# Kernel optimization log

Measured on AMD Instinct MI355X. Metric: run time of the kernel, lower is better.

Reference implementation:

```python
import jax, jax.numpy as jnp
import numpy as np
from jax import lax

B, D, H, W = 4, 64, 64, 64
CH = 150


def setup_inputs() -> dict:
    key = jax.random.key(0)
    k1, k2, k3, k4 = jax.random.split(key, 4)
    image = jax.random.uniform(k1, (B, 2, D, H, W), dtype=jnp.float32)
    # PyTorch-like init scales
    h_w = jax.random.normal(k2, (CH, 1, 3, 3, 3), dtype=jnp.float32) * (1.0 / np.sqrt(27.0))
    h_b = jax.random.normal(k3, (CH,), dtype=jnp.float32) * 0.05
    p_w = jax.random.normal(k4, (1, CH, 1, 1, 1), dtype=jnp.float32) * (1.0 / np.sqrt(CH))
    return {"image": image, "h_w": h_w, "h_b": h_b, "p_w": p_w, "k": 30}


def _max_pool3(v):
    # 3x3x3 max pool, stride 1, padding 1 (torch pads with -inf for max pool)
    return lax.reduce_window(
        v, -jnp.inf, lax.max,
        window_dimensions=(1, 1, 3, 3, 3),
        window_strides=(1, 1, 1, 1, 1),
        padding=[(0, 0), (0, 0), (1, 1), (1, 1), (1, 1)])


def reference(image, h_w, h_b, p_w, k):
    x = image[:, 0:1]            # [B,1,D,H,W] occupancy
    r = image[:, 1:2]            # [B,1,D,H,W] reward
    h = lax.conv_general_dilated(
        x, h_w, window_strides=(1, 1, 1), padding="SAME",
        dimension_numbers=("NCDHW", "OIDHW", "NCDHW"))
    h = jax.nn.relu(h + h_b[None, :, None, None, None])  # [B,150,D,H,W]
    # 1x1x1 conv == channel contraction
    p = jax.nn.sigmoid(jnp.einsum("bcdhw,c->bdhw", h, p_w[0, :, 0, 0, 0])[:, None])
    v = r
    for _ in range(k):
        v = jnp.maximum(v, r + p * (_max_pool3(v) - r))
    return v
```

## Files before the change

kernel.cpp:

```cpp
#include <hip/hip_runtime.h>
#include <math.h>

#define NEG_INF (-__builtin_inff())

typedef __attribute__((ext_vector_type(8))) short short8;
typedef __attribute__((ext_vector_type(4))) float f32x4;

__device__ __forceinline__ unsigned f2bf(float f) {
    union { float f; unsigned u; } v; v.f = f;
    return (v.u + 0x7fffu + ((v.u >> 16) & 1u)) >> 16;
}

__device__ __forceinline__ float dpp_shr1(float x) {
    return __int_as_float(__builtin_amdgcn_update_dpp(
        0, __float_as_int(x), 0x111, 0xF, 0xF, true));
}
__device__ __forceinline__ float dpp_shr2(float x) {
    return __int_as_float(__builtin_amdgcn_update_dpp(
        0, __float_as_int(x), 0x112, 0xF, 0xF, true));
}
__device__ __forceinline__ float dpp_shr4(float x) {
    return __int_as_float(__builtin_amdgcn_update_dpp(
        0, __float_as_int(x), 0x114, 0xF, 0xF, true));
}
__device__ __forceinline__ float dpp_shr8(float x) {
    return __int_as_float(__builtin_amdgcn_update_dpp(
        0, __float_as_int(x), 0x118, 0xF, 0xF, true));
}
__device__ __forceinline__ float dpp_shl1(float x) {
    return __int_as_float(__builtin_amdgcn_update_dpp(
        0, __float_as_int(x), 0x101, 0xF, 0xF, true));
}

__global__ __launch_bounds__(256) void pad_kernel(
    const float* __restrict__ img, unsigned short* __restrict__ pad)
{
    int i = blockIdx.x * 256 + threadIdx.x;
    if (i >= 66 * 66 * 66) return;
    int b = blockIdx.y;
    int z = i / 4356;
    int rem = i - z * 4356;
    int y = rem / 66;
    int x = rem - y * 66;
    float v = 0.f;
    if (z >= 1 && z <= 64 && y >= 1 && y <= 64 && x >= 1 && x <= 64)
        v = img[((size_t)b << 19) + ((z - 1) << 12) + ((y - 1) << 6) + (x - 1)];
    pad[(size_t)b * 287496 + i] = (unsigned short)f2bf(v);
}

__global__ __launch_bounds__(256, 4) void gate_mfma(
    const unsigned short* __restrict__ pad,
    const float* __restrict__ hw, const float* __restrict__ hb,
    const float* __restrict__ pw, float* __restrict__ p)
{
    __shared__ int4 Bsh[10 * 64];

    const int lane = threadIdx.x & 63;
    const int col  = lane & 15;
    const int q    = lane >> 4;
    const int wid  = threadIdx.x >> 6;
    const int W    = blockIdx.x * 4 + wid;

    for (int t = wid; t < 10; t += 4) {
        int c = 16 * t + col;
        bool cv = c < 150;
        unsigned hv[8];
        #pragma unroll
        for (int j = 0; j < 8; ++j) {
            int k = 8 * q + j;
            float wv = 0.f;
            if (cv) {
                if (k < 27) wv = hw[c * 27 + k];
                else if (k == 27) wv = hb[c];
            }
            hv[j] = f2bf(wv);
        }
        Bsh[t * 64 + lane] = make_int4(hv[0] | (hv[1] << 16), hv[2] | (hv[3] << 16),
                                       hv[4] | (hv[5] << 16), hv[6] | (hv[7] << 16));
    }
    float pwv[10];
    #pragma unroll
    for (int t = 0; t < 10; ++t) {
        int c = 16 * t + col;
        pwv[t] = (c < 150) ? pw[c] : 0.f;
    }
    __syncthreads();

    int4 bfrag[10];
    #pragma unroll
    for (int t = 0; t < 10; ++t) bfrag[t] = Bsh[t * 64 + lane];

    int offL[8]; unsigned cstA[8]; bool ldA[8];
    #pragma unroll
    for (int j = 0; j < 8; ++j) {
        int k = 8 * q + j;
        int dz = (k * 57) >> 9;
        int rem = k - 9 * dz;
        int dy = (rem * 171) >> 9;
        int dx = rem - 3 * dy;
        ldA[j]  = (k < 27);
        offL[j] = (k < 27) ? (dz * 4356 + dy * 66 + dx) : 0;
        cstA[j] = (k == 27) ? 0x3F80u : 0u;
    }

    int y = W & 63, zz = (W >> 6) & 63, b = W >> 12;
    int rbase = b * 287496 + zz * 4356 + y * 66 + col;

    #pragma unroll 2
    for (int i = 0; i < 4; ++i) {
        int x0    = i << 4;
        int abase = rbase + x0;

        unsigned av[8];
        #pragma unroll
        for (int j = 0; j < 8; ++j) {
            unsigned v = pad[abase + offL[j]];
            av[j] = ldA[j] ? v : cstA[j];
        }
        union { int4 i4; short8 s8; } af, bfu;
        af.i4 = make_int4(av[0] | (av[1] << 16), av[2] | (av[3] << 16),
                          av[4] | (av[5] << 16), av[6] | (av[7] << 16));

        const f32x4 zero = {0.f, 0.f, 0.f, 0.f};
        f32x4 rr[10];
        #pragma unroll
        for (int t = 0; t < 10; ++t) {
            bfu.i4 = bfrag[t];
            rr[t] = __builtin_amdgcn_mfma_f32_16x16x32_bf16(af.s8, bfu.s8, zero, 0, 0, 0);
        }
        float ax = 0.f, ay = 0.f, az = 0.f, aw = 0.f;
        #pragma unroll
        for (int t = 0; t < 10; ++t) {
            ax = fmaf(pwv[t], fmaxf(rr[t].x, 0.f), ax);
            ay = fmaf(pwv[t], fmaxf(rr[t].y, 0.f), ay);
            az = fmaf(pwv[t], fmaxf(rr[t].z, 0.f), az);
            aw = fmaf(pwv[t], fmaxf(rr[t].w, 0.f), aw);
        }
        ax += dpp_shr1(ax); ax += dpp_shr2(ax); ax += dpp_shr4(ax); ax += dpp_shr8(ax);
        ay += dpp_shr1(ay); ay += dpp_shr2(ay); ay += dpp_shr4(ay); ay += dpp_shr8(ay);
        az += dpp_shr1(az); az += dpp_shr2(az); az += dpp_shr4(az); az += dpp_shr8(az);
        aw += dpp_shr1(aw); aw += dpp_shr2(aw); aw += dpp_shr4(aw); aw += dpp_shr8(aw);
        if (col == 15) {
            float4 o;
            o.x = 1.f / (1.f + __expf(-ax));
            o.y = 1.f / (1.f + __expf(-ay));
            o.z = 1.f / (1.f + __expf(-az));
            o.w = 1.f / (1.f + __expf(-aw));
            *(float4*)(p + (b << 18) + (zz << 12) + (y << 6) + x0 + 4 * q) = o;
        }
    }
}

#define YC2 14
#define PL2 896
#define HALF 5

template<int T>
__global__ __launch_bounds__(448, 3) void prop_kernel(
    const float* __restrict__ vin, int sstride,
    const float* __restrict__ rimg,
    const float* __restrict__ pbuf,
    float* __restrict__ vout)
{
    __shared__ float TL[8 * PL2];
    __shared__ float VEX[2 * PL2];

    int blk = blockIdx.x;
    int b  = blk >> 7;
    int tz = ((blk >> 3) & 15) << 2;
    int ty = (blk & 7) << 3;

    const float* vb = vin  + (size_t)b * sstride;
    const float* rb = rimg + ((size_t)b << 19);
    const float* pb = pbuf + ((size_t)b << 18);
    float*       ob = vout + ((size_t)b << 18);

    int tid  = threadIdx.x;
    int h    = (tid >= 224);
    int t2   = tid - h * 224;
    int x4   = t2 & 15, x0 = x4 << 2;
    int yy   = t2 >> 4;

    int gy = ty + yy - 3;
    bool vy = (unsigned)gy < 64u;
    int lbase = yy * 64 + x0;
    int goff  = gy * 64 + x0;

    float4 v[HALF];
    #pragma unroll
    for (int zi = 0; zi < HALF; ++zi) {
        int z  = h ? (9 - zi) : zi;
        int gz = tz + z - 3;
        float4 val = make_float4(NEG_INF, NEG_INF, NEG_INF, NEG_INF);
        if (vy && ((unsigned)gz < 64u)) val = *(const float4*)(vb + (gz << 12) + goff);
        v[zi] = val;
    }
    *(float4*)(VEX + h * PL2 + lbase) = v[HALF - 1];
    __syncthreads();

    #pragma unroll
    for (int it = 0; it < T; ++it) {
        const int lo = 4 - T + it;
        bool act_t = (yy >= lo - 1) && (yy < 15 - lo);
        bool act   = (yy >= lo) && (yy < YC2 - lo);

        float4 vexN = *(const float4*)(VEX + (h ^ 1) * PL2 + lbase);
        float4 t[4];
        #pragma unroll
        for (int zi = lo; zi < HALF; ++zi) {
            float4 za = v[zi - 1];
            float4 zb = v[zi];
            float4 zc = (zi == HALF - 1) ? vexN : v[zi + 1];
            float4 zm;
            zm.x = fmaxf(fmaxf(za.x, zb.x), zc.x);
            zm.y = fmaxf(fmaxf(za.y, zb.y), zc.y);
            zm.z = fmaxf(fmaxf(za.z, zb.z), zc.z);
            zm.w = fmaxf(fmaxf(za.w, zb.w), zc.w);
            float lm = dpp_shr1(zm.w);
            float rm = dpp_shl1(zm.x);
            if (x4 == 0)  lm = NEG_INF;
            if (x4 == 15) rm = NEG_INF;
            float4 tt;
            tt.x = fmaxf(lm, fmaxf(zm.x, zm.y));
            tt.y = fmaxf(zm.x, fmaxf(zm.y, zm.z));
            tt.z = fmaxf(zm.y, fmaxf(zm.z, zm.w));
            tt.w = fmaxf(fmaxf(zm.z, zm.w), rm);
            t[zi - lo] = tt;
            int z = h ? (9 - zi) : zi;
            if (act_t) *(float4*)(TL + (z - 1) * PL2 + lbase) = tt;
        }
        __syncthreads();

        #pragma unroll
        for (int zi = lo; zi < HALF; ++zi) {
            int z  = h ? (9 - zi) : zi;
            int gz = tz + z - 3;
            if (act) {
                const float* tp = TL + (z - 1) * PL2 + lbase;
                float4 tu = *(const float4*)(tp - 64);
                float4 td = *(const float4*)(tp + 64);
                float4 ts = t[zi - lo];
                float4 m3;
                m3.x = fmaxf(fmaxf(tu.x, td.x), ts.x);
                m3.y = fmaxf(fmaxf(tu.y, td.y), ts.y);
                m3.z = fmaxf(fmaxf(tu.z, td.z), ts.z);
                m3.w = fmaxf(fmaxf(tu.w, td.w), ts.w);
                if (vy && ((unsigned)gz < 64u)) {
                    int off = (gz << 12) + goff;
                    float4 pv = *(const float4*)(pb + off);
                    float4 rv = *(const float4*)(rb + off);
                    float4 nv;
                    nv.x = fmaxf(v[zi].x, fmaf(pv.x, m3.x - rv.x, rv.x));
                    nv.y = fmaxf(v[zi].y, fmaf(pv.y, m3.y - rv.y, rv.y));
                    nv.z = fmaxf(v[zi].z, fmaf(pv.z, m3.z - rv.z, rv.z));
                    nv.w = fmaxf(v[zi].w, fmaf(pv.w, m3.w - rv.w, rv.w));
                    v[zi] = nv;
                    if (it == T - 1) *(float4*)(ob + off) = nv;
                }
            }
        }
        *(float4*)(VEX + h * PL2 + lbase) = v[HALF - 1];
        __syncthreads();
    }
}

extern "C" void kernel_launch(void* const* d_in, const int* in_sizes, int n_in,
                              void* d_out, int out_size, void* d_ws, size_t ws_size,
                              hipStream_t stream) {
    const float* img = (const float*)d_in[0];
    const float* hw  = (const float*)d_in[1];
    const float* hb  = (const float*)d_in[2];
    const float* pw  = (const float*)d_in[3];

    float* out = (float*)d_out;
    float* p   = (float*)d_ws;
    float* vA  = (float*)((char*)d_ws + (4u << 20));
    unsigned short* pad = (unsigned short*)((char*)d_ws + (4u << 20));

    pad_kernel<<<dim3(1124, 4), 256, 0, stream>>>(img, pad);
    gate_mfma<<<4096, 256, 0, stream>>>(pad, hw, hb, pw, p);

    const float* r0 = img + (1 << 18);

    prop_kernel<3><<<512, 448, 0, stream>>>(r0,  1 << 19, r0, p, vA);
    prop_kernel<3><<<512, 448, 0, stream>>>(vA,  1 << 18, r0, p, out);
    prop_kernel<3><<<512, 448, 0, stream>>>(out, 1 << 18, r0, p, vA);
    prop_kernel<3><<<512, 448, 0, stream>>>(vA,  1 << 18, r0, p, out);
    prop_kernel<3><<<512, 448, 0, stream>>>(out, 1 << 18, r0, p, vA);
    prop_kernel<3><<<512, 448, 0, stream>>>(vA,  1 << 18, r0, p, out);
    prop_kernel<3><<<512, 448, 0, stream>>>(out, 1 << 18, r0, p, vA);
    prop_kernel<3><<<512, 448, 0, stream>>>(vA,  1 << 18, r0, p, out);
    prop_kernel<3><<<512, 448, 0, stream>>>(out, 1 << 18, r0, p, vA);
    prop_kernel<3><<<512, 448, 0, stream>>>(vA,  1 << 18, r0, p, out);
}
```

Before: 179.0 us.

## Replace inter-half z exchange with redundant halo compute and double-buffered tiles

```diff
diff --git a/kernel.cpp b/kernel.cpp
--- a/kernel.cpp
+++ b/kernel.cpp
@@ -153,17 +153,16 @@
 
 #define YC2 14
 #define PL2 896
-#define HALF 5
+#define TLP (8 * PL2)
 
 template<int T>
-__global__ __launch_bounds__(448, 3) void prop_kernel(
+__global__ __launch_bounds__(448, 2) void prop_kernel(
     const float* __restrict__ vin, int sstride,
     const float* __restrict__ rimg,
     const float* __restrict__ pbuf,
     float* __restrict__ vout)
 {
-    __shared__ float TL[8 * PL2];
-    __shared__ float VEX[2 * PL2];
+    __shared__ float TL[2 * TLP];
 
     int blk = blockIdx.x;
     int b  = blk >> 7;
@@ -186,31 +185,30 @@
     int lbase = yy * 64 + x0;
     int goff  = gy * 64 + x0;
 
-    float4 v[HALF];
-    #pragma unroll
-    for (int zi = 0; zi < HALF; ++zi) {
+    float4 v[8];
+    #pragma unroll
+    for (int zi = 0; zi < 8; ++zi) {
         int z  = h ? (9 - zi) : zi;
         int gz = tz + z - 3;
         float4 val = make_float4(NEG_INF, NEG_INF, NEG_INF, NEG_INF);
         if (vy && ((unsigned)gz < 64u)) val = *(const float4*)(vb + (gz << 12) + goff);
         v[zi] = val;
     }
-    *(float4*)(VEX + h * PL2 + lbase) = v[HALF - 1];
-    __syncthreads();
-
+
+    int cur = 0;
     #pragma unroll
     for (int it = 0; it < T; ++it) {
-        const int lo = 4 - T + it;
+        const int lo = 1 + it;
+        const int hi = 6 - it;
         bool act_t = (yy >= lo - 1) && (yy < 15 - lo);
         bool act   = (yy >= lo) && (yy < YC2 - lo);
 
-        float4 vexN = *(const float4*)(VEX + (h ^ 1) * PL2 + lbase);
-        float4 t[4];
-        #pragma unroll
-        for (int zi = lo; zi < HALF; ++zi) {
+        float4 t[6];
+        #pragma unroll
+        for (int zi = lo; zi <= hi; ++zi) {
             float4 za = v[zi - 1];
             float4 zb = v[zi];
-            float4 zc = (zi == HALF - 1) ? vexN : v[zi + 1];
+            float4 zc = v[zi + 1];
             float4 zm;
             zm.x = fmaxf(fmaxf(za.x, zb.x), zc.x);
             zm.y = fmaxf(fmaxf(za.y, zb.y), zc.y);
@@ -225,21 +223,23 @@
             tt.y = fmaxf(zm.x, fmaxf(zm.y, zm.z));
             tt.z = fmaxf(zm.y, fmaxf(zm.z, zm.w));
             tt.w = fmaxf(fmaxf(zm.z, zm.w), rm);
-            t[zi - lo] = tt;
-            int z = h ? (9 - zi) : zi;
-            if (act_t) *(float4*)(TL + (z - 1) * PL2 + lbase) = tt;
+            t[zi - 1] = tt;
+            if (zi <= 4) {
+                int z = h ? (9 - zi) : zi;
+                if (act_t) *(float4*)(TL + cur * TLP + (z - 1) * PL2 + lbase) = tt;
+            }
         }
         __syncthreads();
 
         #pragma unroll
-        for (int zi = lo; zi < HALF; ++zi) {
+        for (int zi = lo; zi <= hi; ++zi) {
             int z  = h ? (9 - zi) : zi;
             int gz = tz + z - 3;
             if (act) {
-                const float* tp = TL + (z - 1) * PL2 + lbase;
+                const float* tp = TL + cur * TLP + (z - 1) * PL2 + lbase;
                 float4 tu = *(const float4*)(tp - 64);
                 float4 td = *(const float4*)(tp + 64);
-                float4 ts = t[zi - lo];
+                float4 ts = t[zi - 1];
                 float4 m3;
                 m3.x = fmaxf(fmaxf(tu.x, td.x), ts.x);
                 m3.y = fmaxf(fmaxf(tu.y, td.y), ts.y);
@@ -259,8 +259,7 @@
                 }
             }
         }
-        *(float4*)(VEX + h * PL2 + lbase) = v[HALF - 1];
-        __syncthreads();
+        cur ^= 1;
     }
 }
 
```

New measurement: 184.5 us. +3.1%, slower.

## Fold projection weights into conv weights with sign-sorted channels in gate kernel

Applied to the files above, without the earlier changes.

```diff
diff --git a/kernel.cpp b/kernel.cpp
--- a/kernel.cpp
+++ b/kernel.cpp
@@ -14,18 +14,6 @@
 __device__ __forceinline__ float dpp_shr1(float x) {
     return __int_as_float(__builtin_amdgcn_update_dpp(
         0, __float_as_int(x), 0x111, 0xF, 0xF, true));
-}
-__device__ __forceinline__ float dpp_shr2(float x) {
-    return __int_as_float(__builtin_amdgcn_update_dpp(
-        0, __float_as_int(x), 0x112, 0xF, 0xF, true));
-}
-__device__ __forceinline__ float dpp_shr4(float x) {
-    return __int_as_float(__builtin_amdgcn_update_dpp(
-        0, __float_as_int(x), 0x114, 0xF, 0xF, true));
-}
-__device__ __forceinline__ float dpp_shr8(float x) {
-    return __int_as_float(__builtin_amdgcn_update_dpp(
-        0, __float_as_int(x), 0x118, 0xF, 0xF, true));
 }
 __device__ __forceinline__ float dpp_shl1(float x) {
     return __int_as_float(__builtin_amdgcn_update_dpp(
@@ -48,47 +36,63 @@
     pad[(size_t)b * 287496 + i] = (unsigned short)f2bf(v);
 }
 
-__global__ __launch_bounds__(256, 4) void gate_mfma(
+__global__ __launch_bounds__(256) void prep_kernel(
+    const float* __restrict__ hw, const float* __restrict__ hb,
+    const float* __restrict__ pw, int4* __restrict__ wfrag, int* __restrict__ bnp)
+{
+    __shared__ float pwl[160];
+    __shared__ int   perml[160];
+    int tid = threadIdx.x;
+    if (tid < 160) pwl[tid] = (tid < 150) ? pw[tid] : 0.f;
+    __syncthreads();
+    if (tid < 160) {
+        int Bn = 0;
+        for (int c = 0; c < 150; ++c) Bn += (pwl[c] < 0.f) ? 1 : 0;
+        if (tid == 0) bnp[0] = Bn;
+        int orig = -1;
+        if (tid < Bn) {
+            int cnt = 0;
+            for (int c = 0; c < 150; ++c) if (pwl[c] < 0.f) { if (cnt == tid) { orig = c; break; } ++cnt; }
+        } else if (tid < 150) {
+            int want = tid - Bn, cnt = 0;
+            for (int c = 0; c < 150; ++c) if (!(pwl[c] < 0.f)) { if (cnt == want) { orig = c; break; } ++cnt; }
+        }
+        perml[tid] = orig;
+    }
+    __syncthreads();
+    for (int idx = tid; idx < 640; idx += 256) {
+        int t = idx >> 6, lane = idx & 63;
+        int col = lane & 15, q = lane >> 4;
+        int s = 16 * t + col;
+        int orig = perml[s];
+        unsigned hv[8];
+        #pragma unroll
+        for (int j = 0; j < 8; ++j) {
+            int k = 8 * q + j;
+            float wv = 0.f;
+            if (orig >= 0) {
+                if (k < 27) wv = pwl[orig] * hw[orig * 27 + k];
+                else if (k == 27) wv = pwl[orig] * hb[orig];
+            }
+            hv[j] = f2bf(wv);
+        }
+        wfrag[t * 64 + lane] = make_int4(hv[0] | (hv[1] << 16), hv[2] | (hv[3] << 16),
+                                         hv[4] | (hv[5] << 16), hv[6] | (hv[7] << 16));
+    }
+}
+
+__global__ __launch_bounds__(256, 2) void gate_mfma(
     const unsigned short* __restrict__ pad,
-    const float* __restrict__ hw, const float* __restrict__ hb,
-    const float* __restrict__ pw, float* __restrict__ p)
+    const int4* __restrict__ wfrag, const int* __restrict__ bnp,
+    float* __restrict__ p)
 {
-    __shared__ int4 Bsh[10 * 64];
-
     const int lane = threadIdx.x & 63;
     const int col  = lane & 15;
     const int q    = lane >> 4;
     const int wid  = threadIdx.x >> 6;
     const int W    = blockIdx.x * 4 + wid;
 
-    for (int t = wid; t < 10; t += 4) {
-        int c = 16 * t + col;
-        bool cv = c < 150;
-        unsigned hv[8];
-        #pragma unroll
-        for (int j = 0; j < 8; ++j) {
-            int k = 8 * q + j;
-            float wv = 0.f;
-            if (cv) {
-                if (k < 27) wv = hw[c * 27 + k];
-                else if (k == 27) wv = hb[c];
-            }
-            hv[j] = f2bf(wv);
-        }
-        Bsh[t * 64 + lane] = make_int4(hv[0] | (hv[1] << 16), hv[2] | (hv[3] << 16),
-                                       hv[4] | (hv[5] << 16), hv[6] | (hv[7] << 16));
-    }
-    float pwv[10];
-    #pragma unroll
-    for (int t = 0; t < 10; ++t) {
-        int c = 16 * t + col;
-        pwv[t] = (c < 150) ? pw[c] : 0.f;
-    }
-    __syncthreads();
-
-    int4 bfrag[10];
-    #pragma unroll
-    for (int t = 0; t < 10; ++t) bfrag[t] = Bsh[t * 64 + lane];
+    const int Bn = __builtin_amdgcn_readfirstlane(bnp[0]);
 
     int offL[8]; unsigned cstA[8]; bool ldA[8];
     #pragma unroll
@@ -106,47 +110,70 @@
     int y = W & 63, zz = (W >> 6) & 63, b = W >> 12;
     int rbase = b * 287496 + zz * 4356 + y * 66 + col;
 
-    #pragma unroll 2
-    for (int i = 0; i < 4; ++i) {
-        int x0    = i << 4;
-        int abase = rbase + x0;
-
+    int4 af[4];
+    #pragma unroll
+    for (int g = 0; g < 4; ++g) {
+        int abase = rbase + (g << 4);
         unsigned av[8];
         #pragma unroll
         for (int j = 0; j < 8; ++j) {
             unsigned v = pad[abase + offL[j]];
             av[j] = ldA[j] ? v : cstA[j];
         }
-        union { int4 i4; short8 s8; } af, bfu;
-        af.i4 = make_int4(av[0] | (av[1] << 16), av[2] | (av[3] << 16),
+        af[g] = make_int4(av[0] | (av[1] << 16), av[2] | (av[3] << 16),
                           av[4] | (av[5] << 16), av[6] | (av[7] << 16));
-
-        const f32x4 zero = {0.f, 0.f, 0.f, 0.f};
-        f32x4 rr[10];
-        #pragma unroll
-        for (int t = 0; t < 10; ++t) {
-            bfu.i4 = bfrag[t];
-            rr[t] = __builtin_amdgcn_mfma_f32_16x16x32_bf16(af.s8, bfu.s8, zero, 0, 0, 0);
-        }
-        float ax = 0.f, ay = 0.f, az = 0.f, aw = 0.f;
-        #pragma unroll
-        for (int t = 0; t < 10; ++t) {
-            ax = fmaf(pwv[t], fmaxf(rr[t].x, 0.f), ax);
-            ay = fmaf(pwv[t], fmaxf(rr[t].y, 0.f), ay);
-            az = fmaf(pwv[t], fmaxf(rr[t].z, 0.f), az);
-            aw = fmaf(pwv[t], fmaxf(rr[t].w, 0.f), aw);
-        }
-        ax += dpp_shr1(ax); ax += dpp_shr2(ax); ax += dpp_shr4(ax); ax += dpp_shr8(ax);
-        ay += dpp_shr1(ay); ay += dpp_shr2(ay); ay += dpp_shr4(ay); ay += dpp_shr8(ay);
-        az += dpp_shr1(az); az += dpp_shr2(az); az += dpp_shr4(az); az += dpp_shr8(az);
-        aw += dpp_shr1(aw); aw += dpp_shr2(aw); aw += dpp_shr4(aw); aw += dpp_shr8(aw);
-        if (col == 15) {
-            float4 o;
-            o.x = 1.f / (1.f + __expf(-ax));
-            o.y = 1.f / (1.f + __expf(-ay));
-            o.z = 1.f / (1.f + __expf(-az));
-            o.w = 1.f / (1.f + __expf(-aw));
-            *(float4*)(p + (b << 18) + (zz << 12) + (y << 6) + x0 + 4 * q) = o;
+    }
+
+    const f32x4 zero = {0.f, 0.f, 0.f, 0.f};
+    f32x4 acc[4];
+    #pragma unroll
+    for (int g = 0; g < 4; ++g) acc[g] = zero;
+
+    #pragma unroll
+    for (int t = 0; t < 10; ++t) {
+        union { int4 i4; short8 s8; } wf; wf.i4 = wfrag[t * 64 + lane];
+        f32x4 rr[4];
+        #pragma unroll
+        for (int g = 0; g < 4; ++g) {
+            union { int4 i4; short8 s8; } afu; afu.i4 = af[g];
+            rr[g] = __builtin_amdgcn_mfma_f32_16x16x32_bf16(wf.s8, afu.s8, zero, 0, 0, 0);
+        }
+        if (16 * (t + 1) <= Bn) {
+            #pragma unroll
+            for (int g = 0; g < 4; ++g) {
+                acc[g].x += fminf(rr[g].x, 0.f);
+                acc[g].y += fminf(rr[g].y, 0.f);
+                acc[g].z += fminf(rr[g].z, 0.f);
+                acc[g].w += fminf(rr[g].w, 0.f);
+            }
+        } else if (16 * t >= Bn) {
+            #pragma unroll
+            for (int g = 0; g < 4; ++g) {
+                acc[g].x += fmaxf(rr[g].x, 0.f);
+                acc[g].y += fmaxf(rr[g].y, 0.f);
+                acc[g].z += fmaxf(rr[g].z, 0.f);
+                acc[g].w += fmaxf(rr[g].w, 0.f);
+            }
+        } else {
+            int c0 = 16 * t + 4 * q;
+            #pragma unroll
+            for (int g = 0; g < 4; ++g) {
+                acc[g].x += (c0 + 0 < Bn) ? fminf(rr[g].x, 0.f) : fmaxf(rr[g].x, 0.f);
+                acc[g].y += (c0 + 1 < Bn) ? fminf(rr[g].y, 0.f) : fmaxf(rr[g].y, 0.f);
+                acc[g].z += (c0 + 2 < Bn) ? fminf(rr[g].z, 0.f) : fmaxf(rr[g].z, 0.f);
+                acc[g].w += (c0 + 3 < Bn) ? fminf(rr[g].w, 0.f) : fmaxf(rr[g].w, 0.f);
+            }
+        }
+    }
+
+    #pragma unroll
+    for (int g = 0; g < 4; ++g) {
+        float s = (acc[g].x + acc[g].y) + (acc[g].z + acc[g].w);
+        s += __shfl_xor(s, 16);
+        s += __shfl_xor(s, 32);
+        if (lane < 16) {
+            float o = 1.f / (1.f + __expf(-s));
+            p[(b << 18) + (zz << 12) + (y << 6) + (g << 4) + lane] = o;
         }
     }
 }
@@ -276,9 +303,12 @@
     float* p   = (float*)d_ws;
     float* vA  = (float*)((char*)d_ws + (4u << 20));
     unsigned short* pad = (unsigned short*)((char*)d_ws + (4u << 20));
-
+    int4* wfrag = (int4*)((char*)d_ws + (4u << 20) + 2375680u);
+    int*  bnp   = (int*) ((char*)d_ws + (4u << 20) + 2375680u + 10240u);
+
+    prep_kernel<<<1, 256, 0, stream>>>(hw, hb, pw, wfrag, bnp);
     pad_kernel<<<dim3(1124, 4), 256, 0, stream>>>(img, pad);
-    gate_mfma<<<4096, 256, 0, stream>>>(pad, hw, hb, pw, p);
+    gate_mfma<<<4096, 256, 0, stream>>>(pad, wfrag, bnp, p);
 
     const float* r0 = img + (1 << 18);
 
```

Measured after the change: 196.1 us. 1.1x slower.
